# Kernel optimization log

Hardware: AMD Instinct MI355X
Metric: run time of the kernel (lower is better)

## Reference

```python
import jax, jax.numpy as jnp
import numpy as np

B, P, C_IN, K = 8, 8192, 64, 32
MLP = (64, 64, 128)
BN_EPS = 1e-5


def setup_inputs() -> dict:
    key = jax.random.key(0)
    ks = jax.random.split(key, 2 + len(MLP))
    xyz = jax.random.normal(ks[0], (B, P, 3), jnp.float32)
    feats = jax.random.normal(ks[1], (B, C_IN, P), jnp.float32)
    params = {}
    c = C_IN + 3
    for i, oc in enumerate(MLP):
        params[f"W{i+1}"] = jax.random.normal(ks[2 + i], (oc, c), jnp.float32) * (1.0 / np.sqrt(c))
        params[f"b{i+1}"] = jnp.zeros((oc,), jnp.float32)
        params[f"g{i+1}"] = jnp.ones((oc,), jnp.float32)
        params[f"beta{i+1}"] = jnp.zeros((oc,), jnp.float32)
        c = oc
    return {"xyz": xyz, "feats": feats, **params}


def _conv_bn_relu(x, W, b, g, beta):
    # x: (B, M, K, Cin); 1x1 Conv1d == channel matmul, BN (training mode)
    # over the (B*M, K) "batch x length" axes per output channel.
    y = jnp.einsum('bmkc,oc->bmko', x, W) + b
    mu = jnp.mean(y, axis=(0, 1, 2), keepdims=True)
    var = jnp.var(y, axis=(0, 1, 2), keepdims=True)  # biased var, as torch BN train
    return jax.nn.relu((y - mu) * jax.lax.rsqrt(var + BN_EPS) * g + beta)


def reference(xyz, feats, W1, b1, g1, beta1, W2, b2, g2, beta2, W3, b3, g3, beta3):
    Bb, Pp, _ = xyz.shape
    M = max(1, Pp // 4)
    # torch.linspace(0, P-1, M, dtype=long): float linspace truncated to int
    idx_c = jnp.linspace(0.0, Pp - 1, M).astype(jnp.int32)
    centers = xyz[:, idx_c, :]  # (B, M, 3)
    # squared euclidean distance (same kNN ordering as torch.cdist)
    d2 = (jnp.sum(centers * centers, -1)[:, :, None]
          + jnp.sum(xyz * xyz, -1)[:, None, :]
          - 2.0 * jnp.einsum('bmd,bpd->bmp', centers, xyz))
    _, idx = jax.lax.top_k(-d2, min(K, Pp))  # (B, M, K) nearest indices

    gather = jax.vmap(lambda pts, i: pts[i])  # (P, C), (M, K) -> (M, K, C)
    neigh_xyz = gather(xyz, idx)                      # (B, M, K, 3)
    local_xyz = neigh_xyz - centers[:, :, None, :]
    neigh_f = gather(jnp.swapaxes(feats, 1, 2), idx)  # (B, M, K, C_IN)
    x = jnp.concatenate([local_xyz, neigh_f], axis=-1)  # (B, M, K, 3+C_IN)

    for W, b, g, be in ((W1, b1, g1, beta1), (W2, b2, g2, beta2), (W3, b3, g3, beta3)):
        x = _conv_bn_relu(x, W, b, g, be)

    out = jnp.max(x, axis=2)          # max over K -> (B, M, C_out)
    out = jnp.swapaxes(out, 1, 2)     # (B, C_out, M)
    return centers, out
```

## Files before the change

### kernel.cpp

```cpp
#include <hip/hip_runtime.h>

#define B_ 8
#define P_ 8192
#define M_ 2048
#define K_ 32
#define CIN_ 64
#define C3_ 128
#define BM_ (B_*M_)
#define NTOT_f 524288.0f
#define BN_EPS_ 1e-5f
#define POOLCAP 128
#define XW_STR 112
#define W3_STR 72

typedef __attribute__((ext_vector_type(8))) short bf16x8;
typedef __attribute__((ext_vector_type(4))) float f32x4;

#define WS_FT    (BM_*K_)
#define WS_Y3MAX (WS_FT + B_*P_*CIN_)
#define WS_Y3MIN (WS_Y3MAX + BM_*C3_)
#define WS_STATS (WS_Y3MIN + BM_*C3_)

__device__ inline int center_index(int m) {
  const double step = (double)(P_ - 1) / (double)(M_ - 1);
  return (m == M_ - 1) ? (P_ - 1) : (int)((double)m * step);
}

__device__ inline unsigned short f2bf(float f) {
  unsigned int u = __float_as_uint(f);
  unsigned int r = (u + 0x7fffu + ((u >> 16) & 1u)) >> 16;
  return (unsigned short)r;
}

__device__ inline float sq3(float a, float b, float c) {
  return __fadd_rn(__fadd_rn(__fmul_rn(a, a), __fmul_rn(b, b)), __fmul_rn(c, c));
}

__global__ __launch_bounds__(256) void k_transpose(const float* __restrict__ feats,
                                                   float* __restrict__ ftT) {
  __shared__ float tile[64][65];
  int b = blockIdx.x >> 7;
  int p0 = (blockIdx.x & 127) << 6;
  const float* fb = feats + (size_t)b * CIN_ * P_;
  float* ob = ftT + (size_t)b * P_ * CIN_;
  for (int i = threadIdx.x; i < 64 * 64; i += 256) {
    int c = i >> 6, pp = i & 63;
    tile[c][pp] = fb[c * P_ + p0 + pp];
  }
  __syncthreads();
  for (int i = threadIdx.x; i < 64 * 64; i += 256) {
    int pp = i >> 6, c = i & 63;
    ob[(size_t)(p0 + pp) * CIN_ + c] = tile[c][pp];
  }
}

__device__ inline void cmpx_elem(float& v, int& ix, int i, int size, int d) {
  float pv = __shfl_xor(v, d);
  int pi = __shfl_xor(ix, d);
  bool up = ((i & size) == 0);
  bool lower = ((i & d) == 0);
  bool less = (v < pv) || (v == pv && ix < pi);
  bool keep = (lower == up) ? less : !less;
  if (!keep) { v = pv; ix = pi; }
}

__device__ void pool_compact(float* pv_, int* pi_, int& pc, float& kth, int lane) {
  __threadfence_block();
  float v0 = (lane < pc) ? pv_[lane] : __builtin_inff();
  int   i0 = (lane < pc) ? pi_[lane] : 0x7fffffff;
  float v1 = (lane + 64 < pc) ? pv_[lane + 64] : __builtin_inff();
  int   i1 = (lane + 64 < pc) ? pi_[lane + 64] : 0x7fffffff;
  for (int size = 2; size <= 128; size <<= 1) {
    if (size == 128) {
      bool less = (v0 < v1) || (v0 == v1 && i0 < i1);
      if (!less) { float tv = v0; v0 = v1; v1 = tv; int ti = i0; i0 = i1; i1 = ti; }
    }
    for (int d = (size == 128 ? 32 : (size >> 1)); d >= 1; d >>= 1) {
      cmpx_elem(v0, i0, lane, size, d);
      cmpx_elem(v1, i1, lane + 64, size, d);
    }
  }
  if (lane < 32) { pv_[lane] = v0; pi_[lane] = i0; }
  __threadfence_block();
  pc = 32;
  kth = __shfl(v0, 31);
}

__global__ __launch_bounds__(256) void k_knn(const float* __restrict__ xyz,
                                             float* __restrict__ centers_out,
                                             int* __restrict__ knn_idx) {
  __shared__ float pvals[4][4][POOLCAP];
  __shared__ int   pidxs[4][4][POOLCAP];
  const int w = threadIdx.x >> 6, lane = threadIdx.x & 63;
  const int gw = blockIdx.x * 4 + w;
  const int cid0 = gw * 4;
  const int b = cid0 >> 11;
  const float* xyzb = xyz + (size_t)b * P_ * 3;

  float cx[4], cy[4], cz[4], ccs[4], kth[4];
  int pc[4];
  #pragma unroll
  for (int cc = 0; cc < 4; cc++) {
    int m = (cid0 + cc) & (M_ - 1);
    int ci = center_index(m);
    cx[cc] = xyzb[ci * 3 + 0];
    cy[cc] = xyzb[ci * 3 + 1];
    cz[cc] = xyzb[ci * 3 + 2];
    ccs[cc] = sq3(cx[cc], cy[cc], cz[cc]);
    kth[cc] = __builtin_inff();
    pc[cc] = 0;
  }
  if (lane < 12) {
    int cc = lane / 3, c = lane % 3;
    int m = (cid0 + cc) & (M_ - 1);
    int ci = center_index(m);
    centers_out[(size_t)(cid0 + cc) * 3 + c] = xyzb[ci * 3 + c];
  }

  for (int bi = 0; bi < P_ / 64; bi++) {
    int p = bi * 64 + lane;
    float px = xyzb[p * 3 + 0], py = xyzb[p * 3 + 1], pz = xyzb[p * 3 + 2];
    float pp = sq3(px, py, pz);
    #pragma unroll
    for (int cc = 0; cc < 4; cc++) {
      float dot = __fmul_rn(cx[cc], px);
      dot = __builtin_fmaf(cy[cc], py, dot);
      dot = __builtin_fmaf(cz[cc], pz, dot);
      float d2 = __fsub_rn(__fadd_rn(ccs[cc], pp), __fmul_rn(2.0f, dot));
      bool pass = d2 < kth[cc];
      unsigned long long mask = __ballot(pass);
      if (mask) {
        int cnt = __popcll(mask);
        if (pc[cc] + cnt > POOLCAP)
          pool_compact(&pvals[w][cc][0], &pidxs[w][cc][0], pc[cc], kth[cc], lane);
        int rank = __popcll(mask & ((1ull << lane) - 1ull));
        if (pass) {
          pvals[w][cc][pc[cc] + rank] = d2;
          pidxs[w][cc][pc[cc] + rank] = p;
        }
        pc[cc] += cnt;
      }
    }
  }
  #pragma unroll
  for (int cc = 0; cc < 4; cc++) {
    pool_compact(&pvals[w][cc][0], &pidxs[w][cc][0], pc[cc], kth[cc], lane);
    if (lane < K_) knn_idx[(size_t)(cid0 + cc) * K_ + lane] = pidxs[w][cc][lane];
  }
}

__device__ inline void gather_mfma(const float* __restrict__ xyz,
                                   const float* __restrict__ ftT,
                                   const int* __restrict__ knn,
                                   int cid, int lane,
                                   unsigned short* __restrict__ xq) {
  const int b = cid >> 11;
  const int m = cid & (M_ - 1);
  const int ci = center_index(m);
  const float* xyzb = xyz + (size_t)b * P_ * 3;
  const int r = lane >> 1, hf = lane & 1;
  const int p = knn[(size_t)cid * K_ + r];
  const float* frow = ftT + ((size_t)b * P_ + p) * CIN_ + hf * 32;
  unsigned short* row = xq + r * XW_STR;
  #pragma unroll
  for (int i = 0; i < 8; i++) {
    float4 v = *(const float4*)(frow + i * 4);
    ushort4 u = make_ushort4(f2bf(v.x), f2bf(v.y), f2bf(v.z), f2bf(v.w));
    *(ushort4*)(row + hf * 32 + i * 4) = u;
  }
  if (hf == 0) {
    float dx = xyzb[p * 3 + 0] - xyzb[ci * 3 + 0];
    float dy = xyzb[p * 3 + 1] - xyzb[ci * 3 + 1];
    float dz = xyzb[p * 3 + 2] - xyzb[ci * 3 + 2];
    ushort4 u = make_ushort4(f2bf(dx), f2bf(dy), f2bf(dz), 0);
    *(ushort4*)(row + 64) = u;
  } else {
    ushort4 z = make_ushort4(0, 0, 0, 0);
    #pragma unroll
    for (int i = 0; i < 7; i++) *(ushort4*)(row + 68 + i * 4) = z;
  }
}

__device__ inline void load_w1_frags(const float* __restrict__ W1, int lane, bf16x8 (&w1f)[4][3]) {
  const int o16 = lane & 15, q = lane >> 4;
  #pragma unroll
  for (int nt = 0; nt < 4; nt++) {
    const float* wr = W1 + (nt * 16 + o16) * 67;
    #pragma unroll
    for (int s = 0; s < 3; s++) {
      bf16x8 f;
      #pragma unroll
      for (int j = 0; j < 8; j++) {
        int c = s * 32 + q * 8 + j;
        float v = (c < 64) ? wr[c + 3] : ((c < 67) ? wr[c - 64] : 0.0f);
        f[j] = (short)f2bf(v);
      }
      w1f[nt][s] = f;
    }
  }
}

__device__ inline void load_w2_frags(const float* __restrict__ W2, int lane, bf16x8 (&w2f)[4][2]) {
  const int o16 = lane & 15, q = lane >> 4;
  #pragma unroll
  for (int nt = 0; nt < 4; nt++) {
    const float* wr = W2 + (nt * 16 + o16) * 64;
    #pragma unroll
    for (int s = 0; s < 2; s++) {
      bf16x8 f;
      #pragma unroll
      for (int j = 0; j < 8; j++) f[j] = (short)f2bf(wr[s * 32 + q * 8 + j]);
      w2f[nt][s] = f;
    }
  }
}

__device__ inline bf16x8 lds_afrag(const unsigned short* __restrict__ xq, int mt, int s, int lane) {
  return *(const bf16x8*)(xq + (mt * 16 + (lane & 15)) * XW_STR + s * 32 + (lane >> 4) * 8);
}

__global__ __launch_bounds__(256, 3) void k_mf1(const float* __restrict__ xyz,
                                                const float* __restrict__ ftT,
                                                const int* __restrict__ knn,
                                                const float* __restrict__ W1,
                                                const float* __restrict__ b1,
                                                float* __restrict__ stats) {
  __shared__ __align__(16) unsigned short xw[4][32 * XW_STR];
  __shared__ float sld[128];
  const int t = threadIdx.x, w = t >> 6, lane = t & 63, o16 = lane & 15;
  if (t < 128) sld[t] = 0.0f;

  bf16x8 w1f[4][3];
  load_w1_frags(W1, lane, w1f);
  float b1l[4], sacc[4], qacc[4];
  #pragma unroll
  for (int nt = 0; nt < 4; nt++) { b1l[nt] = b1[nt * 16 + o16]; sacc[nt] = 0.f; qacc[nt] = 0.f; }
  __syncthreads();

  unsigned short* xq = &xw[w][0];
  const int cid0 = blockIdx.x * 32 + w * 8;
  for (int n = 0; n < 8; n++) {
    gather_mfma(xyz, ftT, knn, cid0 + n, lane, xq);
    f32x4 acc[2][4];
    #pragma unroll
    for (int mt = 0; mt < 2; mt++)
      #pragma unroll
      for (int nt = 0; nt < 4; nt++) acc[mt][nt] = (f32x4){0.f, 0.f, 0.f, 0.f};
    #pragma unroll
    for (int s = 0; s < 3; s++) {
      bf16x8 a0 = lds_afrag(xq, 0, s, lane);
      bf16x8 a1 = lds_afrag(xq, 1, s, lane);
      #pragma unroll
      for (int nt = 0; nt < 4; nt++) {
        acc[0][nt] = __builtin_amdgcn_mfma_f32_16x16x32_bf16(a0, w1f[nt][s], acc[0][nt], 0, 0, 0);
        acc[1][nt] = __builtin_amdgcn_mfma_f32_16x16x32_bf16(a1, w1f[nt][s], acc[1][nt], 0, 0, 0);
      }
    }
    #pragma unroll
    for (int nt = 0; nt < 4; nt++)
      #pragma unroll
      for (int mt = 0; mt < 2; mt++)
        #pragma unroll
        for (int rr = 0; rr < 4; rr++) {
          float y = acc[mt][nt][rr] + b1l[nt];
          sacc[nt] += y;
          qacc[nt] = fmaf(y, y, qacc[nt]);
        }
  }
  #pragma unroll
  for (int nt = 0; nt < 4; nt++) {
    float s = sacc[nt]; s += __shfl_xor(s, 16); s += __shfl_xor(s, 32);
    float qq = qacc[nt]; qq += __shfl_xor(qq, 16); qq += __shfl_xor(qq, 32);
    if (lane < 16) { atomicAdd(&sld[nt * 16 + lane], s); atomicAdd(&sld[64 + nt * 16 + lane], qq); }
  }
  __syncthreads();
  if (t < 64) { atomicAdd(&stats[t], sld[t]); atomicAdd(&stats[64 + t], sld[64 + t]); }
}

__global__ __launch_bounds__(256, 2) void k_mf2(const float* __restrict__ xyz,
                                                const float* __restrict__ ftT,
                                                const int* __restrict__ knn,
                                                const float* __restrict__ W1,
                                                const float* __restrict__ b1,
                                                const float* __restrict__ g1,
                                                const float* __restrict__ be1,
                                                const float* __restrict__ W2,
                                                const float* __restrict__ b2,
                                                float* __restrict__ stats) {
  __shared__ __align__(16) unsigned short xw[4][32 * XW_STR];
  __shared__ float sld[128];
  const int t = threadIdx.x, w = t >> 6, lane = t & 63, o16 = lane & 15, q = lane >> 4;
  if (t < 128) sld[t] = 0.0f;

  bf16x8 w1f[4][3];
  bf16x8 w2f[4][2];
  load_w1_frags(W1, lane, w1f);
  load_w2_frags(W2, lane, w2f);
  float b1l[4], sc1l[4], sh1l[4], b2l[4], sacc[4], qacc[4];
  #pragma unroll
  for (int nt = 0; nt < 4; nt++) {
    int o = nt * 16 + o16;
    float mean = stats[o] * (1.0f / NTOT_f);
    float var = stats[64 + o] * (1.0f / NTOT_f) - mean * mean;
    float rs = rsqrtf(var + BN_EPS_);
    sc1l[nt] = g1[o] * rs;
    sh1l[nt] = be1[o] - mean * sc1l[nt];
    b1l[nt] = b1[o];
    b2l[nt] = b2[o];
    sacc[nt] = 0.f; qacc[nt] = 0.f;
  }
  __syncthreads();

  unsigned short* xq = &xw[w][0];
  const int cid0 = blockIdx.x * 32 + w * 8;
  for (int n = 0; n < 8; n++) {
    gather_mfma(xyz, ftT, knn, cid0 + n, lane, xq);
    f32x4 acc[2][4];
    #pragma unroll
    for (int mt = 0; mt < 2; mt++)
      #pragma unroll
      for (int nt = 0; nt < 4; nt++) acc[mt][nt] = (f32x4){0.f, 0.f, 0.f, 0.f};
    #pragma unroll
    for (int s = 0; s < 3; s++) {
      bf16x8 a0 = lds_afrag(xq, 0, s, lane);
      bf16x8 a1 = lds_afrag(xq, 1, s, lane);
      #pragma unroll
      for (int nt = 0; nt < 4; nt++) {
        acc[0][nt] = __builtin_amdgcn_mfma_f32_16x16x32_bf16(a0, w1f[nt][s], acc[0][nt], 0, 0, 0);
        acc[1][nt] = __builtin_amdgcn_mfma_f32_16x16x32_bf16(a1, w1f[nt][s], acc[1][nt], 0, 0, 0);
      }
    }
    #pragma unroll
    for (int nt = 0; nt < 4; nt++)
      #pragma unroll
      for (int mt = 0; mt < 2; mt++)
        #pragma unroll
        for (int rr = 0; rr < 4; rr++) {
          float y = acc[mt][nt][rr] + b1l[nt];
          float h = fmaxf(fmaf(y, sc1l[nt], sh1l[nt]), 0.0f);
          xq[(mt * 16 + q * 4 + rr) * XW_STR + nt * 16 + o16] = f2bf(h);
        }
    f32x4 acc2[2][4];
    #pragma unroll
    for (int mt = 0; mt < 2; mt++)
      #pragma unroll
      for (int nt = 0; nt < 4; nt++) acc2[mt][nt] = (f32x4){0.f, 0.f, 0.f, 0.f};
    #pragma unroll
    for (int s = 0; s < 2; s++) {
      bf16x8 a0 = lds_afrag(xq, 0, s, lane);
      bf16x8 a1 = lds_afrag(xq, 1, s, lane);
      #pragma unroll
      for (int nt = 0; nt < 4; nt++) {
        acc2[0][nt] = __builtin_amdgcn_mfma_f32_16x16x32_bf16(a0, w2f[nt][s], acc2[0][nt], 0, 0, 0);
        acc2[1][nt] = __builtin_amdgcn_mfma_f32_16x16x32_bf16(a1, w2f[nt][s], acc2[1][nt], 0, 0, 0);
      }
    }
    #pragma unroll
    for (int nt = 0; nt < 4; nt++)
      #pragma unroll
      for (int mt = 0; mt < 2; mt++)
        #pragma unroll
        for (int rr = 0; rr < 4; rr++) {
          float y = acc2[mt][nt][rr] + b2l[nt];
          sacc[nt] += y;
          qacc[nt] = fmaf(y, y, qacc[nt]);
        }
  }
  #pragma unroll
  for (int nt = 0; nt < 4; nt++) {
    float s = sacc[nt]; s += __shfl_xor(s, 16); s += __shfl_xor(s, 32);
    float qq = qacc[nt]; qq += __shfl_xor(qq, 16); qq += __shfl_xor(qq, 32);
    if (lane < 16) { atomicAdd(&sld[nt * 16 + lane], s); atomicAdd(&sld[64 + nt * 16 + lane], qq); }
  }
  __syncthreads();
  if (t < 64) { atomicAdd(&stats[128 + t], sld[t]); atomicAdd(&stats[192 + t], sld[64 + t]); }
}

__global__ __launch_bounds__(256, 2) void k_mf3(const float* __restrict__ xyz,
                                                const float* __restrict__ ftT,
                                                const int* __restrict__ knn,
                                                const float* __restrict__ W1,
                                                const float* __restrict__ b1,
                                                const float* __restrict__ g1,
                                                const float* __restrict__ be1,
                                                const float* __restrict__ W2,
                                                const float* __restrict__ b2,
                                                const float* __restrict__ g2,
                                                const float* __restrict__ be2,
                                                const float* __restrict__ W3,
                                                const float* __restrict__ b3,
                                                float* __restrict__ stats,
                                                float* __restrict__ y3max,
                                                float* __restrict__ y3min) {
  __shared__ __align__(16) unsigned short xw[4][32 * XW_STR];
  __shared__ __align__(16) unsigned short ws3[128 * W3_STR];
  __shared__ float sld[256];
  const int t = threadIdx.x, w = t >> 6, lane = t & 63, o16 = lane & 15, q = lane >> 4;
  if (t < 256) sld[t] = 0.0f;
  for (int i = t; i < 128 * 64; i += 256) {
    int o = i >> 6, c = i & 63;
    ws3[o * W3_STR + c] = f2bf(W3[i]);
  }

  bf16x8 w1f[4][3];
  bf16x8 w2f[4][2];
  load_w1_frags(W1, lane, w1f);
  load_w2_frags(W2, lane, w2f);
  float b1l[4], sc1l[4], sh1l[4], b2l[4], sc2l[4], sh2l[4];
  #pragma unroll
  for (int nt = 0; nt < 4; nt++) {
    int o = nt * 16 + o16;
    float mean = stats[o] * (1.0f / NTOT_f);
    float var = stats[64 + o] * (1.0f / NTOT_f) - mean * mean;
    float rs = rsqrtf(var + BN_EPS_);
    sc1l[nt] = g1[o] * rs;
    sh1l[nt] = be1[o] - mean * sc1l[nt];
    b1l[nt] = b1[o];
    float mean2 = stats[128 + o] * (1.0f / NTOT_f);
    float var2 = stats[192 + o] * (1.0f / NTOT_f) - mean2 * mean2;
    float rs2 = rsqrtf(var2 + BN_EPS_);
    sc2l[nt] = g2[o] * rs2;
    sh2l[nt] = be2[o] - mean2 * sc2l[nt];
    b2l[nt] = b2[o];
  }
  float b3l[8], sacc[8], qacc[8];
  #pragma unroll
  for (int nt = 0; nt < 8; nt++) { b3l[nt] = b3[nt * 16 + o16]; sacc[nt] = 0.f; qacc[nt] = 0.f; }
  __syncthreads();

  unsigned short* xq = &xw[w][0];
  const int cid0 = blockIdx.x * 32 + w * 8;
  for (int n = 0; n < 8; n++) {
    const int cid = cid0 + n;
    gather_mfma(xyz, ftT, knn, cid, lane, xq);
    f32x4 acc[2][4];
    #pragma unroll
    for (int mt = 0; mt < 2; mt++)
      #pragma unroll
      for (int nt = 0; nt < 4; nt++) acc[mt][nt] = (f32x4){0.f, 0.f, 0.f, 0.f};
    #pragma unroll
    for (int s = 0; s < 3; s++) {
      bf16x8 a0 = lds_afrag(xq, 0, s, lane);
      bf16x8 a1 = lds_afrag(xq, 1, s, lane);
      #pragma unroll
      for (int nt = 0; nt < 4; nt++) {
        acc[0][nt] = __builtin_amdgcn_mfma_f32_16x16x32_bf16(a0, w1f[nt][s], acc[0][nt], 0, 0, 0);
        acc[1][nt] = __builtin_amdgcn_mfma_f32_16x16x32_bf16(a1, w1f[nt][s], acc[1][nt], 0, 0, 0);
      }
    }
    #pragma unroll
    for (int nt = 0; nt < 4; nt++)
      #pragma unroll
      for (int mt = 0; mt < 2; mt++)
        #pragma unroll
        for (int rr = 0; rr < 4; rr++) {
          float y = acc[mt][nt][rr] + b1l[nt];
          float h = fmaxf(fmaf(y, sc1l[nt], sh1l[nt]), 0.0f);
          xq[(mt * 16 + q * 4 + rr) * XW_STR + nt * 16 + o16] = f2bf(h);
        }
    #pragma unroll
    for (int mt = 0; mt < 2; mt++)
      #pragma unroll
      for (int nt = 0; nt < 4; nt++) acc[mt][nt] = (f32x4){0.f, 0.f, 0.f, 0.f};
    #pragma unroll
    for (int s = 0; s < 2; s++) {
      bf16x8 a0 = lds_afrag(xq, 0, s, lane);
      bf16x8 a1 = lds_afrag(xq, 1, s, lane);
      #pragma unroll
      for (int nt = 0; nt < 4; nt++) {
        acc[0][nt] = __builtin_amdgcn_mfma_f32_16x16x32_bf16(a0, w2f[nt][s], acc[0][nt], 0, 0, 0);
        acc[1][nt] = __builtin_amdgcn_mfma_f32_16x16x32_bf16(a1, w2f[nt][s], acc[1][nt], 0, 0, 0);
      }
    }
    #pragma unroll
    for (int nt = 0; nt < 4; nt++)
      #pragma unroll
      for (int mt = 0; mt < 2; mt++)
        #pragma unroll
        for (int rr = 0; rr < 4; rr++) {
          float y = acc[mt][nt][rr] + b2l[nt];
          float h = fmaxf(fmaf(y, sc2l[nt], sh2l[nt]), 0.0f);
          xq[(mt * 16 + q * 4 + rr) * XW_STR + nt * 16 + o16] = f2bf(h);
        }
    f32x4 acc3[2][8];
    #pragma unroll
    for (int mt = 0; mt < 2; mt++)
      #pragma unroll
      for (int nt = 0; nt < 8; nt++) acc3[mt][nt] = (f32x4){0.f, 0.f, 0.f, 0.f};
    #pragma unroll
    for (int s = 0; s < 2; s++) {
      bf16x8 a0 = lds_afrag(xq, 0, s, lane);
      bf16x8 a1 = lds_afrag(xq, 1, s, lane);
      #pragma unroll
      for (int nt = 0; nt < 8; nt++) {
        bf16x8 bf = *(const bf16x8*)(ws3 + (nt * 16 + o16) * W3_STR + s * 32 + q * 8);
        acc3[0][nt] = __builtin_amdgcn_mfma_f32_16x16x32_bf16(a0, bf, acc3[0][nt], 0, 0, 0);
        acc3[1][nt] = __builtin_amdgcn_mfma_f32_16x16x32_bf16(a1, bf, acc3[1][nt], 0, 0, 0);
      }
    }
    #pragma unroll
    for (int nt = 0; nt < 8; nt++) {
      float mx = -__builtin_inff(), mn = __builtin_inff();
      #pragma unroll
      for (int mt = 0; mt < 2; mt++)
        #pragma unroll
        for (int rr = 0; rr < 4; rr++) {
          float y = acc3[mt][nt][rr] + b3l[nt];
          sacc[nt] += y;
          qacc[nt] = fmaf(y, y, qacc[nt]);
          mx = fmaxf(mx, y);
          mn = fminf(mn, y);
        }
      mx = fmaxf(mx, __shfl_xor(mx, 16)); mx = fmaxf(mx, __shfl_xor(mx, 32));
      mn = fminf(mn, __shfl_xor(mn, 16)); mn = fminf(mn, __shfl_xor(mn, 32));
      if (lane < 16) {
        y3max[(size_t)cid * C3_ + nt * 16 + lane] = mx;
        y3min[(size_t)cid * C3_ + nt * 16 + lane] = mn;
      }
    }
  }
  #pragma unroll
  for (int nt = 0; nt < 8; nt++) {
    float s = sacc[nt]; s += __shfl_xor(s, 16); s += __shfl_xor(s, 32);
    float qq = qacc[nt]; qq += __shfl_xor(qq, 16); qq += __shfl_xor(qq, 32);
    if (lane < 16) { atomicAdd(&sld[nt * 16 + lane], s); atomicAdd(&sld[128 + nt * 16 + lane], qq); }
  }
  __syncthreads();
  if (t < 128) { atomicAdd(&stats[256 + t], sld[t]); atomicAdd(&stats[384 + t], sld[128 + t]); }
}

__global__ __launch_bounds__(256) void k_out(const float* __restrict__ y3max,
                                             const float* __restrict__ y3min,
                                             const float* __restrict__ stats,
                                             const float* __restrict__ g3,
                                             const float* __restrict__ be3,
                                             float* __restrict__ outp) {
  __shared__ float sc[128], sh[128];
  const int t = threadIdx.x;
  if (t < 128) {
    float mean = stats[256 + t] * (1.0f / NTOT_f);
    float var = stats[384 + t] * (1.0f / NTOT_f) - mean * mean;
    float rs = rsqrtf(var + BN_EPS_);
    float s = g3[t] * rs;
    sc[t] = s;
    sh[t] = be3[t] - mean * s;
  }
  __syncthreads();
  int gid = blockIdx.x * 256 + t;
  int m = gid & (M_ - 1);
  int o = (gid >> 11) & 127;
  int b = gid >> 18;
  float s = sc[o], h = sh[o];
  size_t src = ((size_t)(b * M_ + m)) * C3_ + o;
  float v = (s >= 0.0f) ? y3max[src] : y3min[src];
  outp[gid] = fmaxf(fmaf(v, s, h), 0.0f);
}

extern "C" void kernel_launch(void* const* d_in, const int* in_sizes, int n_in,
                              void* d_out, int out_size, void* d_ws, size_t ws_size,
                              hipStream_t stream) {
  const float* xyz  = (const float*)d_in[0];
  const float* feats = (const float*)d_in[1];
  const float* W1 = (const float*)d_in[2];
  const float* b1 = (const float*)d_in[3];
  const float* g1 = (const float*)d_in[4];
  const float* be1 = (const float*)d_in[5];
  const float* W2 = (const float*)d_in[6];
  const float* b2 = (const float*)d_in[7];
  const float* g2 = (const float*)d_in[8];
  const float* be2 = (const float*)d_in[9];
  const float* W3 = (const float*)d_in[10];
  const float* b3 = (const float*)d_in[11];
  const float* g3 = (const float*)d_in[12];
  const float* be3 = (const float*)d_in[13];

  float* out = (float*)d_out;
  float* centers = out;
  float* outp = out + (size_t)B_ * M_ * 3;

  float* wsf = (float*)d_ws;
  int* idx = (int*)wsf;
  float* ftT = wsf + WS_FT;
  float* y3max = wsf + WS_Y3MAX;
  float* y3min = wsf + WS_Y3MIN;
  float* stats = wsf + WS_STATS;

  hipMemsetAsync(stats, 0, 512 * sizeof(float), stream);
  k_transpose<<<1024, 256, 0, stream>>>(feats, ftT);
  k_knn<<<1024, 256, 0, stream>>>(xyz, centers, idx);
  k_mf1<<<512, 256, 0, stream>>>(xyz, ftT, idx, W1, b1, stats);
  k_mf2<<<512, 256, 0, stream>>>(xyz, ftT, idx, W1, b1, g1, be1, W2, b2, stats);
  k_mf3<<<512, 256, 0, stream>>>(xyz, ftT, idx, W1, b1, g1, be1, W2, b2, g2, be2,
                                 W3, b3, stats, y3max, y3min);
  k_out<<<8192, 256, 0, stream>>>(y3max, y3min, stats, g3, be3, outp);
}
```

Before: 431.0 us.

## Cache layer-2 pre-BN activations in bf16 to skip recompute in layer 3

k_mf2 now writes its layer-2 pre-BN outputs as bf16 into a workspace buffer when the workspace is large enough. A new kernel k_mf3f reads that buffer, applies BN2 and ReLU, and runs the layer-3 MFMA, max/min pooling and stats. This avoids re-gathering the neighbours and recomputing layers 1 and 2 in the third pass. The cost is writing and reading a 64 MB bf16 intermediate, plus an extra bf16 rounding of y2 before normalisation. It falls back to the old k_mf3 when the workspace is too small.

```diff
diff --git a/kernel.cpp b/kernel.cpp
--- a/kernel.cpp
+++ b/kernel.cpp
@@ -6,7 +6,7 @@
 #define K_ 32
 #define CIN_ 64
 #define C3_ 128
-#define BM_ (B_*M_)
+#define BM_ (B_*P_/4)
 #define NTOT_f 524288.0f
 #define BN_EPS_ 1e-5f
 #define POOLCAP 128
@@ -20,6 +20,7 @@
 #define WS_Y3MAX (WS_FT + B_*P_*CIN_)
 #define WS_Y3MIN (WS_Y3MAX + BM_*C3_)
 #define WS_STATS (WS_Y3MIN + BM_*C3_)
+#define WS_Y2F   (WS_STATS + 512)
 
 __device__ inline int center_index(int m) {
   const double step = (double)(P_ - 1) / (double)(M_ - 1);
@@ -30,6 +31,9 @@
   unsigned int u = __float_as_uint(f);
   unsigned int r = (u + 0x7fffu + ((u >> 16) & 1u)) >> 16;
   return (unsigned short)r;
+}
+__device__ inline float bf2f(unsigned short s) {
+  return __uint_as_float(((unsigned int)s) << 16);
 }
 
 __device__ inline float sq3(float a, float b, float c) {
@@ -286,7 +290,8 @@
                                                 const float* __restrict__ be1,
                                                 const float* __restrict__ W2,
                                                 const float* __restrict__ b2,
-                                                float* __restrict__ stats) {
+                                                float* __restrict__ stats,
+                                                unsigned short* __restrict__ y2b) {
   __shared__ __align__(16) unsigned short xw[4][32 * XW_STR];
   __shared__ float sld[128];
   const int t = threadIdx.x, w = t >> 6, lane = t & 63, o16 = lane & 15, q = lane >> 4;
@@ -364,7 +369,17 @@
           float y = acc2[mt][nt][rr] + b2l[nt];
           sacc[nt] += y;
           qacc[nt] = fmaf(y, y, qacc[nt]);
+          if (y2b) xq[(mt * 16 + q * 4 + rr) * XW_STR + nt * 16 + o16] = f2bf(y);
         }
+    if (y2b) {
+      unsigned short* dst = y2b + (size_t)(cid0 + n) * 2048;
+      #pragma unroll
+      for (int j = 0; j < 8; j++) {
+        int chunk = j * 64 + lane;
+        int r = chunk >> 4, c = (chunk & 15) * 4;
+        *(ushort4*)(dst + chunk * 4) = *(const ushort4*)(xq + r * XW_STR + c);
+      }
+    }
   }
   #pragma unroll
   for (int nt = 0; nt < 4; nt++) {
@@ -374,6 +389,103 @@
   }
   __syncthreads();
   if (t < 64) { atomicAdd(&stats[128 + t], sld[t]); atomicAdd(&stats[192 + t], sld[64 + t]); }
+}
+
+__global__ __launch_bounds__(256, 2) void k_mf3f(const unsigned short* __restrict__ y2b,
+                                                 const float* __restrict__ g2,
+                                                 const float* __restrict__ be2,
+                                                 const float* __restrict__ W3,
+                                                 const float* __restrict__ b3,
+                                                 float* __restrict__ stats,
+                                                 float* __restrict__ y3max,
+                                                 float* __restrict__ y3min) {
+  __shared__ __align__(16) unsigned short xw[4][32 * XW_STR];
+  __shared__ __align__(16) unsigned short ws3[128 * W3_STR];
+  __shared__ float sld[256];
+  __shared__ __align__(16) float sc2s[64], sh2s[64];
+  const int t = threadIdx.x, w = t >> 6, lane = t & 63, o16 = lane & 15, q = lane >> 4;
+  if (t < 256) sld[t] = 0.0f;
+  for (int i = t; i < 128 * 64; i += 256) {
+    int o = i >> 6, c = i & 63;
+    ws3[o * W3_STR + c] = f2bf(W3[i]);
+  }
+  if (t < 64) {
+    float mean2 = stats[128 + t] * (1.0f / NTOT_f);
+    float var2 = stats[192 + t] * (1.0f / NTOT_f) - mean2 * mean2;
+    float rs2 = rsqrtf(var2 + BN_EPS_);
+    float sc = g2[t] * rs2;
+    sc2s[t] = sc;
+    sh2s[t] = be2[t] - mean2 * sc;
+  }
+  float b3l[8], sacc[8], qacc[8];
+  #pragma unroll
+  for (int nt = 0; nt < 8; nt++) { b3l[nt] = b3[nt * 16 + o16]; sacc[nt] = 0.f; qacc[nt] = 0.f; }
+  __syncthreads();
+
+  unsigned short* xq = &xw[w][0];
+  const int cid0 = blockIdx.x * 32 + w * 8;
+  for (int n = 0; n < 8; n++) {
+    const int cid = cid0 + n;
+    const unsigned short* src = y2b + (size_t)cid * 2048;
+    #pragma unroll
+    for (int j = 0; j < 8; j++) {
+      int chunk = j * 64 + lane;
+      int r = chunk >> 4, c = (chunk & 15) * 4;
+      ushort4 u = *(const ushort4*)(src + chunk * 4);
+      float4 sc4 = *(const float4*)(&sc2s[c]);
+      float4 sh4 = *(const float4*)(&sh2s[c]);
+      ushort4 h;
+      h.x = f2bf(fmaxf(fmaf(bf2f(u.x), sc4.x, sh4.x), 0.0f));
+      h.y = f2bf(fmaxf(fmaf(bf2f(u.y), sc4.y, sh4.y), 0.0f));
+      h.z = f2bf(fmaxf(fmaf(bf2f(u.z), sc4.z, sh4.z), 0.0f));
+      h.w = f2bf(fmaxf(fmaf(bf2f(u.w), sc4.w, sh4.w), 0.0f));
+      *(ushort4*)(xq + r * XW_STR + c) = h;
+    }
+    f32x4 acc3[2][8];
+    #pragma unroll
+    for (int mt = 0; mt < 2; mt++)
+      #pragma unroll
+      for (int nt = 0; nt < 8; nt++) acc3[mt][nt] = (f32x4){0.f, 0.f, 0.f, 0.f};
+    #pragma unroll
+    for (int s = 0; s < 2; s++) {
+      bf16x8 a0 = lds_afrag(xq, 0, s, lane);
+      bf16x8 a1 = lds_afrag(xq, 1, s, lane);
+      #pragma unroll
+      for (int nt = 0; nt < 8; nt++) {
+        bf16x8 bf = *(const bf16x8*)(ws3 + (nt * 16 + o16) * W3_STR + s * 32 + q * 8);
+        acc3[0][nt] = __builtin_amdgcn_mfma_f32_16x16x32_bf16(a0, bf, acc3[0][nt], 0, 0, 0);
+        acc3[1][nt] = __builtin_amdgcn_mfma_f32_16x16x32_bf16(a1, bf, acc3[1][nt], 0, 0, 0);
+      }
+    }
+    #pragma unroll
+    for (int nt = 0; nt < 8; nt++) {
+      float mx = -__builtin_inff(), mn = __builtin_inff();
+      #pragma unroll
+      for (int mt = 0; mt < 2; mt++)
+        #pragma unroll
+        for (int rr = 0; rr < 4; rr++) {
+          float y = acc3[mt][nt][rr] + b3l[nt];
+          sacc[nt] += y;
+          qacc[nt] = fmaf(y, y, qacc[nt]);
+          mx = fmaxf(mx, y);
+          mn = fminf(mn, y);
+        }
+      mx = fmaxf(mx, __shfl_xor(mx, 16)); mx = fmaxf(mx, __shfl_xor(mx, 32));
+      mn = fminf(mn, __shfl_xor(mn, 16)); mn = fminf(mn, __shfl_xor(mn, 32));
+      if (lane < 16) {
+        y3max[(size_t)cid * C3_ + nt * 16 + lane] = mx;
+        y3min[(size_t)cid * C3_ + nt * 16 + lane] = mn;
+      }
+    }
+  }
+  #pragma unroll
+  for (int nt = 0; nt < 8; nt++) {
+    float s = sacc[nt]; s += __shfl_xor(s, 16); s += __shfl_xor(s, 32);
+    float qq = qacc[nt]; qq += __shfl_xor(qq, 16); qq += __shfl_xor(qq, 32);
+    if (lane < 16) { atomicAdd(&sld[nt * 16 + lane], s); atomicAdd(&sld[128 + nt * 16 + lane], qq); }
+  }
+  __syncthreads();
+  if (t < 128) { atomicAdd(&stats[256 + t], sld[t]); atomicAdd(&stats[384 + t], sld[128 + t]); }
 }
 
 __global__ __launch_bounds__(256, 2) void k_mf3(const float* __restrict__ xyz,
@@ -584,13 +696,21 @@
   float* y3max = wsf + WS_Y3MAX;
   float* y3min = wsf + WS_Y3MIN;
   float* stats = wsf + WS_STATS;
+  unsigned short* y2b = (unsigned short*)(wsf + WS_Y2F);
+  const size_t need = (size_t)WS_Y2F * 4 + (size_t)BM_ * K_ * CIN_ * 2;
+  const bool useY2 = ws_size >= need;
 
   hipMemsetAsync(stats, 0, 512 * sizeof(float), stream);
   k_transpose<<<1024, 256, 0, stream>>>(feats, ftT);
   k_knn<<<1024, 256, 0, stream>>>(xyz, centers, idx);
   k_mf1<<<512, 256, 0, stream>>>(xyz, ftT, idx, W1, b1, stats);
-  k_mf2<<<512, 256, 0, stream>>>(xyz, ftT, idx, W1, b1, g1, be1, W2, b2, stats);
-  k_mf3<<<512, 256, 0, stream>>>(xyz, ftT, idx, W1, b1, g1, be1, W2, b2, g2, be2,
-                                 W3, b3, stats, y3max, y3min);
+  k_mf2<<<512, 256, 0, stream>>>(xyz, ftT, idx, W1, b1, g1, be1, W2, b2, stats,
+                                 useY2 ? y2b : (unsigned short*)nullptr);
+  if (useY2) {
+    k_mf3f<<<512, 256, 0, stream>>>(y2b, g2, be2, W3, b3, stats, y3max, y3min);
+  } else {
+    k_mf3<<<512, 256, 0, stream>>>(xyz, ftT, idx, W1, b1, g1, be1, W2, b2, g2, be2,
+                                   W3, b3, stats, y3max, y3min);
+  }
   k_out<<<8192, 256, 0, stream>>>(y3max, y3min, stats, g3, be3, outp);
 }
```

New measurement: 402.4 us. 6.6% less time.

## Split kNN scan across wave pairs and cache layer-2 output for layer 3

Applied to the files above, without the earlier changes.

The kNN kernel now has two waves share each group of four centers. Each wave scans half of the points, and the two sorted top-32 lists are merged with a shuffle-based bitonic merge. This doubles the parallelism of the dominant scan. Separately, k_mf2 now writes the pre-BN layer-2 activations as bf16 to workspace, so the third-layer kernel reads them back instead of re-gathering and recomputing layers 1 and 2. That trades recomputation for about 64 MB of extra memory traffic and adds a bf16 rounding of y before BN.

```diff
diff --git a/kernel.cpp b/kernel.cpp
--- a/kernel.cpp
+++ b/kernel.cpp
@@ -20,6 +20,7 @@
 #define WS_Y3MAX (WS_FT + B_*P_*CIN_)
 #define WS_Y3MIN (WS_Y3MAX + BM_*C3_)
 #define WS_STATS (WS_Y3MIN + BM_*C3_)
+#define WS_Y2F   (WS_STATS + 512)
 
 __device__ inline int center_index(int m) {
   const double step = (double)(P_ - 1) / (double)(M_ - 1);
@@ -30,6 +31,9 @@
   unsigned int u = __float_as_uint(f);
   unsigned int r = (u + 0x7fffu + ((u >> 16) & 1u)) >> 16;
   return (unsigned short)r;
+}
+__device__ inline float bf2f(unsigned short s) {
+  return __uint_as_float(((unsigned int)s) << 16);
 }
 
 __device__ inline float sq3(float a, float b, float c) {
@@ -92,8 +96,9 @@
   __shared__ float pvals[4][4][POOLCAP];
   __shared__ int   pidxs[4][4][POOLCAP];
   const int w = threadIdx.x >> 6, lane = threadIdx.x & 63;
-  const int gw = blockIdx.x * 4 + w;
-  const int cid0 = gw * 4;
+  const int gl = w >> 1;
+  const int h  = w & 1;
+  const int cid0 = (blockIdx.x * 2 + gl) * 4;
   const int b = cid0 >> 11;
   const float* xyzb = xyz + (size_t)b * P_ * 3;
 
@@ -110,15 +115,16 @@
     kth[cc] = __builtin_inff();
     pc[cc] = 0;
   }
-  if (lane < 12) {
+  if (h == 0 && lane < 12) {
     int cc = lane / 3, c = lane % 3;
     int m = (cid0 + cc) & (M_ - 1);
     int ci = center_index(m);
     centers_out[(size_t)(cid0 + cc) * 3 + c] = xyzb[ci * 3 + c];
   }
 
-  for (int bi = 0; bi < P_ / 64; bi++) {
-    int p = bi * 64 + lane;
+  const int pbase = h * (P_ / 2);
+  for (int bi = 0; bi < P_ / 128; bi++) {
+    int p = pbase + bi * 64 + lane;
     float px = xyzb[p * 3 + 0], py = xyzb[p * 3 + 1], pz = xyzb[p * 3 + 2];
     float pp = sq3(px, py, pz);
     #pragma unroll
@@ -143,9 +149,29 @@
     }
   }
   #pragma unroll
-  for (int cc = 0; cc < 4; cc++) {
+  for (int cc = 0; cc < 4; cc++)
     pool_compact(&pvals[w][cc][0], &pidxs[w][cc][0], pc[cc], kth[cc], lane);
-    if (lane < K_) knn_idx[(size_t)(cid0 + cc) * K_ + lane] = pidxs[w][cc][lane];
+  __syncthreads();
+
+  #pragma unroll
+  for (int tt = 0; tt < 2; tt++) {
+    int task = w * 2 + tt;
+    int glm = task >> 2, cc = task & 3;
+    int wa = glm * 2, wb = wa + 1;
+    float v;
+    int ix;
+    if (lane < 32) { v = pvals[wa][cc][lane]; ix = pidxs[wa][cc][lane]; }
+    else           { v = pvals[wb][cc][63 - lane]; ix = pidxs[wb][cc][63 - lane]; }
+    #pragma unroll
+    for (int d = 32; d >= 1; d >>= 1) {
+      float pv = __shfl_xor(v, d);
+      int pi = __shfl_xor(ix, d);
+      bool less = (v < pv) || (v == pv && ix < pi);
+      bool keep = ((lane & d) == 0) ? less : !less;
+      if (!keep) { v = pv; ix = pi; }
+    }
+    int cidt = blockIdx.x * 8 + glm * 4 + cc;
+    if (lane < K_) knn_idx[(size_t)cidt * K_ + lane] = ix;
   }
 }
 
@@ -286,7 +312,8 @@
                                                 const float* __restrict__ be1,
                                                 const float* __restrict__ W2,
                                                 const float* __restrict__ b2,
-                                                float* __restrict__ stats) {
+                                                float* __restrict__ stats,
+                                                unsigned short* __restrict__ y2b) {
   __shared__ __align__(16) unsigned short xw[4][32 * XW_STR];
   __shared__ float sld[128];
   const int t = threadIdx.x, w = t >> 6, lane = t & 63, o16 = lane & 15, q = lane >> 4;
@@ -364,7 +391,15 @@
           float y = acc2[mt][nt][rr] + b2l[nt];
           sacc[nt] += y;
           qacc[nt] = fmaf(y, y, qacc[nt]);
+          xq[(mt * 16 + q * 4 + rr) * XW_STR + nt * 16 + o16] = f2bf(y);
         }
+    unsigned short* dst = y2b + (size_t)(cid0 + n) * 2048;
+    #pragma unroll
+    for (int j = 0; j < 8; j++) {
+      int chunk = j * 64 + lane;
+      int r = chunk >> 4, c = (chunk & 15) * 4;
+      *(ushort4*)(dst + chunk * 4) = *(const ushort4*)(xq + r * XW_STR + c);
+    }
   }
   #pragma unroll
   for (int nt = 0; nt < 4; nt++) {
@@ -376,52 +411,31 @@
   if (t < 64) { atomicAdd(&stats[128 + t], sld[t]); atomicAdd(&stats[192 + t], sld[64 + t]); }
 }
 
-__global__ __launch_bounds__(256, 2) void k_mf3(const float* __restrict__ xyz,
-                                                const float* __restrict__ ftT,
-                                                const int* __restrict__ knn,
-                                                const float* __restrict__ W1,
-                                                const float* __restrict__ b1,
-                                                const float* __restrict__ g1,
-                                                const float* __restrict__ be1,
-                                                const float* __restrict__ W2,
-                                                const float* __restrict__ b2,
-                                                const float* __restrict__ g2,
-                                                const float* __restrict__ be2,
-                                                const float* __restrict__ W3,
-                                                const float* __restrict__ b3,
-                                                float* __restrict__ stats,
-                                                float* __restrict__ y3max,
-                                                float* __restrict__ y3min) {
+__global__ __launch_bounds__(256, 2) void k_mf3f(const unsigned short* __restrict__ y2b,
+                                                 const float* __restrict__ g2,
+                                                 const float* __restrict__ be2,
+                                                 const float* __restrict__ W3,
+                                                 const float* __restrict__ b3,
+                                                 float* __restrict__ stats,
+                                                 float* __restrict__ y3max,
+                                                 float* __restrict__ y3min) {
   __shared__ __align__(16) unsigned short xw[4][32 * XW_STR];
   __shared__ __align__(16) unsigned short ws3[128 * W3_STR];
   __shared__ float sld[256];
+  __shared__ __align__(16) float sc2s[64], sh2s[64];
   const int t = threadIdx.x, w = t >> 6, lane = t & 63, o16 = lane & 15, q = lane >> 4;
   if (t < 256) sld[t] = 0.0f;
   for (int i = t; i < 128 * 64; i += 256) {
     int o = i >> 6, c = i & 63;
     ws3[o * W3_STR + c] = f2bf(W3[i]);
   }
-
-  bf16x8 w1f[4][3];
-  bf16x8 w2f[4][2];
-  load_w1_frags(W1, lane, w1f);
-  load_w2_frags(W2, lane, w2f);
-  float b1l[4], sc1l[4], sh1l[4], b2l[4], sc2l[4], sh2l[4];
-  #pragma unroll
-  for (int nt = 0; nt < 4; nt++) {
-    int o = nt * 16 + o16;
-    float mean = stats[o] * (1.0f / NTOT_f);
-    float var = stats[64 + o] * (1.0f / NTOT_f) - mean * mean;
-    float rs = rsqrtf(var + BN_EPS_);
-    sc1l[nt] = g1[o] * rs;
-    sh1l[nt] = be1[o] - mean * sc1l[nt];
-    b1l[nt] = b1[o];
-    float mean2 = stats[128 + o] * (1.0f / NTOT_f);
-    float var2 = stats[192 + o] * (1.0f / NTOT_f) - mean2 * mean2;
+  if (t < 64) {
+    float mean2 = stats[128 + t] * (1.0f / NTOT_f);
+    float var2 = stats[192 + t] * (1.0f / NTOT_f) - mean2 * mean2;
     float rs2 = rsqrtf(var2 + BN_EPS_);
-    sc2l[nt] = g2[o] * rs2;
-    sh2l[nt] = be2[o] - mean2 * sc2l[nt];
-    b2l[nt] = b2[o];
+    float sc = g2[t] * rs2;
+    sc2s[t] = sc;
+    sh2s[t] = be2[t] - mean2 * sc;
   }
   float b3l[8], sacc[8], qacc[8];
   #pragma unroll
@@ -432,56 +446,21 @@
   const int cid0 = blockIdx.x * 32 + w * 8;
   for (int n = 0; n < 8; n++) {
     const int cid = cid0 + n;
-    gather_mfma(xyz, ftT, knn, cid, lane, xq);
-    f32x4 acc[2][4];
-    #pragma unroll
-    for (int mt = 0; mt < 2; mt++)
-      #pragma unroll
-      for (int nt = 0; nt < 4; nt++) acc[mt][nt] = (f32x4){0.f, 0.f, 0.f, 0.f};
-    #pragma unroll
-    for (int s = 0; s < 3; s++) {
-      bf16x8 a0 = lds_afrag(xq, 0, s, lane);
-      bf16x8 a1 = lds_afrag(xq, 1, s, lane);
-      #pragma unroll
-      for (int nt = 0; nt < 4; nt++) {
-        acc[0][nt] = __builtin_amdgcn_mfma_f32_16x16x32_bf16(a0, w1f[nt][s], acc[0][nt], 0, 0, 0);
-        acc[1][nt] = __builtin_amdgcn_mfma_f32_16x16x32_bf16(a1, w1f[nt][s], acc[1][nt], 0, 0, 0);
-      }
-    }
-    #pragma unroll
-    for (int nt = 0; nt < 4; nt++)
-      #pragma unroll
-      for (int mt = 0; mt < 2; mt++)
-        #pragma unroll
-        for (int rr = 0; rr < 4; rr++) {
-          float y = acc[mt][nt][rr] + b1l[nt];
-          float h = fmaxf(fmaf(y, sc1l[nt], sh1l[nt]), 0.0f);
-          xq[(mt * 16 + q * 4 + rr) * XW_STR + nt * 16 + o16] = f2bf(h);
-        }
-    #pragma unroll
-    for (int mt = 0; mt < 2; mt++)
-      #pragma unroll
-      for (int nt = 0; nt < 4; nt++) acc[mt][nt] = (f32x4){0.f, 0.f, 0.f, 0.f};
-    #pragma unroll
-    for (int s = 0; s < 2; s++) {
-      bf16x8 a0 = lds_afrag(xq, 0, s, lane);
-      bf16x8 a1 = lds_afrag(xq, 1, s, lane);
-      #pragma unroll
-      for (int nt = 0; nt < 4; nt++) {
-        acc[0][nt] = __builtin_amdgcn_mfma_f32_16x16x32_bf16(a0, w2f[nt][s], acc[0][nt], 0, 0, 0);
-        acc[1][nt] = __builtin_amdgcn_mfma_f32_16x16x32_bf16(a1, w2f[nt][s], acc[1][nt], 0, 0, 0);
-      }
-    }
-    #pragma unroll
-    for (int nt = 0; nt < 4; nt++)
-      #pragma unroll
-      for (int mt = 0; mt < 2; mt++)
-        #pragma unroll
-        for (int rr = 0; rr < 4; rr++) {
-          float y = acc[mt][nt][rr] + b2l[nt];
-          float h = fmaxf(fmaf(y, sc2l[nt], sh2l[nt]), 0.0f);
-          xq[(mt * 16 + q * 4 + rr) * XW_STR + nt * 16 + o16] = f2bf(h);
-        }
+    const unsigned short* src = y2b + (size_t)cid * 2048;
+    #pragma unroll
+    for (int j = 0; j < 8; j++) {
+      int chunk = j * 64 + lane;
+      int r = chunk >> 4, c = (chunk & 15) * 4;
+      ushort4 u = *(const ushort4*)(src + chunk * 4);
+      float4 sc4 = *(const float4*)(&sc2s[c]);
+      float4 sh4 = *(const float4*)(&sh2s[c]);
+      ushort4 h;
+      h.x = f2bf(fmaxf(fmaf(bf2f(u.x), sc4.x, sh4.x), 0.0f));
+      h.y = f2bf(fmaxf(fmaf(bf2f(u.y), sc4.y, sh4.y), 0.0f));
+      h.z = f2bf(fmaxf(fmaf(bf2f(u.z), sc4.z, sh4.z), 0.0f));
+      h.w = f2bf(fmaxf(fmaf(bf2f(u.w), sc4.w, sh4.w), 0.0f));
+      *(ushort4*)(xq + r * XW_STR + c) = h;
+    }
     f32x4 acc3[2][8];
     #pragma unroll
     for (int mt = 0; mt < 2; mt++)
@@ -584,13 +563,13 @@
   float* y3max = wsf + WS_Y3MAX;
   float* y3min = wsf + WS_Y3MIN;
   float* stats = wsf + WS_STATS;
+  unsigned short* y2b = (unsigned short*)(wsf + WS_Y2F);
 
   hipMemsetAsync(stats, 0, 512 * sizeof(float), stream);
   k_transpose<<<1024, 256, 0, stream>>>(feats, ftT);
-  k_knn<<<1024, 256, 0, stream>>>(xyz, centers, idx);
+  k_knn<<<2048, 256, 0, stream>>>(xyz, centers, idx);
   k_mf1<<<512, 256, 0, stream>>>(xyz, ftT, idx, W1, b1, stats);
-  k_mf2<<<512, 256, 0, stream>>>(xyz, ftT, idx, W1, b1, g1, be1, W2, b2, stats);
-  k_mf3<<<512, 256, 0, stream>>>(xyz, ftT, idx, W1, b1, g1, be1, W2, b2, g2, be2,
-                                 W3, b3, stats, y3max, y3min);
+  k_mf2<<<512, 256, 0, stream>>>(xyz, ftT, idx, W1, b1, g1, be1, W2, b2, stats, y2b);
+  k_mf3f<<<512, 256, 0, stream>>>(y2b, g2, be2, W3, b3, stats, y3max, y3min);
   k_out<<<8192, 256, 0, stream>>>(y3max, y3min, stats, g3, be3, outp);
 }
```

Measured after the change: 490.2 us. 1.14x slower.
